# Performance work log

Hardware: AMD Instinct MI355X
Metric: run time of the kernel (lower is better)

The kernel has to match this reference:

```python
import jax, jax.numpy as jnp
import numpy as np

N = 50000      # nodes / stations
E = 600000     # edges
IN = 16        # in_channels
ED = 8         # edge_dim
HID = 128      # hidden
H = 4          # heads
C = HID // H   # 32 per-head channels
EMB = HID // 2 # station embedding dim
FEAT = HID - EMB
SLOPE = 0.2    # GATv2 LeakyReLU negative slope


def setup_inputs() -> dict:
    key = jax.random.key(0)
    ks = jax.random.split(key, 32)
    r = lambda i, shape, s=0.05: (jax.random.normal(ks[i], shape, jnp.float32) * s)
    inp = {
        "x": jax.random.normal(ks[0], (N, IN), jnp.float32),
        "node_idx": jax.random.randint(ks[1], (N,), 0, N),
        "edge_index": jax.random.randint(ks[2], (2, E), 0, N),
        "edge_attr": jax.random.normal(ks[3], (E, ED), jnp.float32),
        # params
        "emb": r(4, (N, EMB)),
        "W_in": r(5, (IN, FEAT)), "b_in": jnp.zeros((FEAT,), jnp.float32),
        # conv1 (GATv2: lin_l, lin_r, lin_edge, att, out bias)
        "Wl1": r(6, (HID, HID)), "bl1": jnp.zeros((HID,), jnp.float32),
        "Wr1": r(7, (HID, HID)), "br1": jnp.zeros((HID,), jnp.float32),
        "We1": r(8, (ED, HID)),  "be1": jnp.zeros((HID,), jnp.float32),
        "att1": r(9, (H, C)),    "bo1": jnp.zeros((HID,), jnp.float32),
        # conv2
        "Wl2": r(10, (HID, HID)), "bl2": jnp.zeros((HID,), jnp.float32),
        "Wr2": r(11, (HID, HID)), "br2": jnp.zeros((HID,), jnp.float32),
        "We2": r(12, (ED, HID)),  "be2": jnp.zeros((HID,), jnp.float32),
        "att2": r(13, (H, C)),    "bo2": jnp.zeros((HID,), jnp.float32),
        # layer norms
        "g1": jnp.ones((HID,), jnp.float32), "beta1": jnp.zeros((HID,), jnp.float32),
        "g2": jnp.ones((HID,), jnp.float32), "beta2": jnp.zeros((HID,), jnp.float32),
        # output head
        "W_out": r(14, (HID, 1)), "b_out": jnp.zeros((1,), jnp.float32),
    }
    return inp


def _gatv2(x, src, dst, ea, Wl, bl, Wr, br, We, be, att, bo):
    # x: [N,HID] -> per-head projections [N,H,C]
    xl = (x @ Wl + bl).reshape(-1, H, C)   # source transform
    xr = (x @ Wr + br).reshape(-1, H, C)   # target transform
    ee = (ea @ We + be).reshape(-1, H, C)  # edge transform [E,H,C]
    s = jax.nn.leaky_relu(xl[src] + xr[dst] + ee, SLOPE)  # [E,H,C]
    logit = jnp.einsum('ehc,hc->eh', s, att)              # [E,H]
    # segment softmax over destination node
    amax = jax.lax.stop_gradient(jax.ops.segment_max(logit, dst, num_segments=N))
    amax = jnp.where(jnp.isfinite(amax), amax, 0.0)
    ex = jnp.exp(logit - amax[dst])
    den = jax.ops.segment_sum(ex, dst, num_segments=N)
    alpha = ex / den[dst]                                  # [E,H]
    out = jax.ops.segment_sum(xl[src] * alpha[..., None], dst, num_segments=N)
    return out.reshape(-1, HID) + bo


def _ln(x, g, b):
    mu = x.mean(-1, keepdims=True)
    v = ((x - mu) ** 2).mean(-1, keepdims=True)
    return (x - mu) * jax.lax.rsqrt(v + 1e-5) * g + b


def reference(x, node_idx, edge_index, edge_attr, emb, W_in, b_in,
              Wl1, bl1, Wr1, br1, We1, be1, att1, bo1,
              Wl2, bl2, Wr2, br2, We2, be2, att2, bo2,
              g1, beta1, g2, beta2, W_out, b_out):
    src, dst = edge_index[0], edge_index[1]
    feat = jax.nn.relu(x @ W_in + b_in)                       # [N,FEAT]
    z = jnp.concatenate([feat, emb[node_idx]], axis=-1)       # [N,HID]
    h = jax.nn.relu(_gatv2(z, src, dst, edge_attr, Wl1, bl1, Wr1, br1, We1, be1, att1, bo1))
    z = _ln(z + h, g1, beta1)
    h = jax.nn.relu(_gatv2(z, src, dst, edge_attr, Wl2, bl2, Wr2, br2, We2, be2, att2, bo2))
    z = _ln(z + h, g2, beta2)
    return (z @ W_out + b_out).squeeze(-1)                    # [N]
```

## Files before the change

kernel.cpp:

```cpp
#include <hip/hip_runtime.h>
#include <hip/hip_bf16.h>

#define NN 50000
#define NE 600000
#define IND 16
#define EDD 8
#define HIDD 128
#define NH 4
#define CC 32
#define EMBD 64
#define FEATD 64
#define NB_SCAN ((NN + 255) / 256)

typedef __hip_bfloat16 bf16;
typedef __attribute__((ext_vector_type(8))) short bshort8;
typedef __attribute__((ext_vector_type(4))) float floatx4;

__device__ __forceinline__ float b2f(bf16 v) { return __bfloat162float(v); }

__device__ __forceinline__ unsigned short f2bu(float f) {
    unsigned int u = __float_as_uint(f);
    u += 0x7fffu + ((u >> 16) & 1u);
    return (unsigned short)(u >> 16);
}

template <bool F32>
__device__ __forceinline__ float LD(const void* p, long long i) {
    if constexpr (F32) return ((const float*)p)[i];
    else return __bfloat162float(((const bf16*)p)[i]);
}

__global__ void k_init0(int* __restrict__ cnt, int* __restrict__ deg) {
    int i = blockIdx.x * blockDim.x + threadIdx.x;
    if (i == 0) *cnt = 0;
    if (i < NN) deg[i] = 0;
}

__global__ void k_detect(const unsigned short* __restrict__ x, int nhalf, int* __restrict__ cnt) {
    __shared__ int c;
    if (threadIdx.x == 0) c = 0;
    __syncthreads();
    int i = blockIdx.x * blockDim.x + threadIdx.x;
    int hits = 0;
    for (; i < nhalf; i += gridDim.x * blockDim.x)
        if ((x[i] & 0x7F80u) == 0x7F80u) hits++;
    if (hits) atomicAdd(&c, hits);
    __syncthreads();
    if (threadIdx.x == 0 && c) atomicAdd(cnt, c);
}

__device__ __forceinline__ bool is_f32(const int* cnt) { return *cnt > 8; }

__global__ void k_hist(const int* __restrict__ ei, int* __restrict__ deg, int* __restrict__ rank) {
    int e = blockIdx.x * blockDim.x + threadIdx.x;
    if (e < NE) rank[e] = atomicAdd(&deg[ei[NE + e]], 1);
}

__global__ void k_scan1(const int* __restrict__ deg, int* __restrict__ off,
                        int* __restrict__ bsum) {
    __shared__ int tile[256];
    int t = threadIdx.x;
    int gid = blockIdx.x * 256 + t;
    int v = (gid < NN) ? deg[gid] : 0;
    tile[t] = v;
    __syncthreads();
    #pragma unroll
    for (int o = 1; o < 256; o <<= 1) {
        int u = (t >= o) ? tile[t - o] : 0;
        __syncthreads();
        tile[t] += u;
        __syncthreads();
    }
    if (gid < NN) off[gid] = tile[t] - v;
    if (t == 255) bsum[blockIdx.x] = tile[255];
}
__global__ void k_scan2(int* __restrict__ bsum) {
    __shared__ int tile[256];
    int t = threadIdx.x;
    int v = (t < NB_SCAN) ? bsum[t] : 0;
    tile[t] = v;
    __syncthreads();
    #pragma unroll
    for (int o = 1; o < 256; o <<= 1) {
        int u = (t >= o) ? tile[t - o] : 0;
        __syncthreads();
        tile[t] += u;
        __syncthreads();
    }
    if (t < NB_SCAN) bsum[t] = tile[t] - v;
}
__global__ void k_scan3(int* __restrict__ off, const int* __restrict__ bsum) {
    int gid = blockIdx.x * 256 + threadIdx.x;
    if (gid < NN) off[gid] += bsum[blockIdx.x];
    if (gid == 0) off[NN] = NE;
}

template <bool F32>
__device__ void fill_impl(const int* __restrict__ ei, const int* __restrict__ off,
                          const int* __restrict__ rank, int* __restrict__ esrc,
                          uint4* __restrict__ ea8, const void* ea) {
    int e = blockIdx.x * blockDim.x + threadIdx.x;
    if (e >= NE) return;
    int slot = off[ei[NE + e]] + rank[e];
    esrc[slot] = ei[e];
    unsigned int w[4];
    #pragma unroll
    for (int d = 0; d < 4; d++) {
        unsigned int lo = f2bu(LD<F32>(ea, (long long)e * EDD + 2 * d));
        unsigned int hi = f2bu(LD<F32>(ea, (long long)e * EDD + 2 * d + 1));
        w[d] = lo | (hi << 16);
    }
    uint4 v; v.x = w[0]; v.y = w[1]; v.z = w[2]; v.w = w[3];
    ea8[slot] = v;
}
__global__ void k_fill(const int* cnt, const int* ei, const int* off, const int* rank,
                       int* esrc, uint4* ea8, const void* ea) {
    if (is_f32(cnt)) fill_impl<true>(ei, off, rank, esrc, ea8, ea);
    else             fill_impl<false>(ei, off, rank, esrc, ea8, ea);
}

template <bool F32>
__device__ void build_z_impl(const void* x, const int* __restrict__ node_idx, const void* emb,
                             const void* W_in, const void* b_in, bf16* __restrict__ zb) {
    int n = blockIdx.x, t = threadIdx.x;
    float val;
    if (t < FEATD) {
        float acc = LD<F32>(b_in, t);
        #pragma unroll
        for (int k = 0; k < IND; k++)
            acc += LD<F32>(x, (long long)n * IND + k) * LD<F32>(W_in, k * FEATD + t);
        val = fmaxf(acc, 0.f);
    } else {
        val = LD<F32>(emb, (long long)node_idx[n] * EMBD + (t - FEATD));
    }
    zb[n * HIDD + t] = __float2bfloat16(val);
}
__global__ void k_build_z(const int* cnt, const void* x, const int* node_idx, const void* emb,
                          const void* W_in, const void* b_in, bf16* zb) {
    if (is_f32(cnt)) build_z_impl<true>(x, node_idx, emb, W_in, b_in, zb);
    else             build_z_impl<false>(x, node_idx, emb, W_in, b_in, zb);
}

template <bool F32>
__device__ void prepw_impl(const void* Wl1, const void* bl1, const void* Wr1, const void* br1,
                           const void* Wl2, const void* bl2, const void* Wr2, const void* br2,
                           bf16* __restrict__ wbT, float* __restrict__ bias) {
    int layer = blockIdx.x >> 8;
    int n = blockIdx.x & 255;
    int k = threadIdx.x;
    const void* W = layer ? (n < HIDD ? Wl2 : Wr2) : (n < HIDD ? Wl1 : Wr1);
    const void* b = layer ? (n < HIDD ? bl2 : br2) : (n < HIDD ? bl1 : br1);
    int nn = n & (HIDD - 1);
    wbT[(layer * 256 + n) * HIDD + k] = __float2bfloat16(LD<F32>(W, k * HIDD + nn));
    if (k == 0) bias[layer * 256 + n] = LD<F32>(b, nn);
}
__global__ void k_prepw(const int* cnt,
                        const void* Wl1, const void* bl1, const void* Wr1, const void* br1,
                        const void* Wl2, const void* bl2, const void* Wr2, const void* br2,
                        bf16* wbT, float* bias) {
    if (is_f32(cnt)) prepw_impl<true>(Wl1, bl1, Wr1, br1, Wl2, bl2, Wr2, br2, wbT, bias);
    else             prepw_impl<false>(Wl1, bl1, Wr1, br1, Wl2, bl2, Wr2, br2, wbT, bias);
}

__global__ __launch_bounds__(256) void k_projmm(const bf16* __restrict__ zb,
                                                const bf16* __restrict__ wbT,
                                                const float* __restrict__ bias,
                                                bf16* __restrict__ xl, bf16* __restrict__ xr) {
    int wave = threadIdx.x >> 6, lane = threadIdx.x & 63;
    int m0 = blockIdx.x * 64;
    int n0 = wave * 64;
    int l15 = lane & 15, q = lane >> 4;
    bshort8 bfr[4][4];
    #pragma unroll
    for (int j = 0; j < 4; j++)
        #pragma unroll
        for (int s = 0; s < 4; s++)
            bfr[j][s] = *(const bshort8*)(wbT + ((n0 + j * 16 + l15) << 7) + s * 32 + q * 8);
    float bv[4];
    #pragma unroll
    for (int j = 0; j < 4; j++) bv[j] = bias[n0 + j * 16 + l15];
    #pragma unroll
    for (int mi = 0; mi < 4; mi++) {
        const bf16* arow = zb + ((long long)(m0 + mi * 16 + l15) << 7) + q * 8;
        floatx4 acc0 = {0.f, 0.f, 0.f, 0.f}, acc1 = acc0, acc2 = acc0, acc3 = acc0;
        #pragma unroll
        for (int s = 0; s < 4; s++) {
            bshort8 a = *(const bshort8*)(arow + s * 32);
            acc0 = __builtin_amdgcn_mfma_f32_16x16x32_bf16(a, bfr[0][s], acc0, 0, 0, 0);
            acc1 = __builtin_amdgcn_mfma_f32_16x16x32_bf16(a, bfr[1][s], acc1, 0, 0, 0);
            acc2 = __builtin_amdgcn_mfma_f32_16x16x32_bf16(a, bfr[2][s], acc2, 0, 0, 0);
            acc3 = __builtin_amdgcn_mfma_f32_16x16x32_bf16(a, bfr[3][s], acc3, 0, 0, 0);
        }
        floatx4 accs[4] = {acc0, acc1, acc2, acc3};
        #pragma unroll
        for (int j = 0; j < 4; j++) {
            int colg = n0 + j * 16 + l15;
            bf16* dst = (colg < HIDD) ? (xl + colg) : (xr + (colg - HIDD));
            #pragma unroll
            for (int r = 0; r < 4; r++) {
                int rowc = m0 + mi * 16 + q * 4 + r;
                if (rowc < NN) dst[(long long)rowc << 7] = __float2bfloat16(accs[j][r] + bv[j]);
            }
        }
    }
}

template <bool F32, bool LAST>
__device__ void gat_impl(const int* __restrict__ off, const int* __restrict__ esrc,
                         const uint4* __restrict__ ea8,
                         const void* We, const void* be, const void* att,
                         const bf16* __restrict__ xl, const bf16* __restrict__ xr,
                         const void* bo, bf16* __restrict__ zb,
                         const void* g, const void* beta,
                         const void* Wo, const void* bout, void* out) {
    int wave = threadIdx.x >> 6;
    int half = (threadIdx.x >> 5) & 1;
    int lane5 = threadIdx.x & 31;
    int n = blockIdx.x * 8 + wave * 2 + half;
    int c0 = lane5 << 2;
    float wv[EDD][4], at[4], bev[4];
    #pragma unroll
    for (int d = 0; d < EDD; d++)
        #pragma unroll
        for (int j = 0; j < 4; j++) wv[d][j] = LD<F32>(We, d * HIDD + c0 + j);
    #pragma unroll
    for (int j = 0; j < 4; j++) {
        at[j] = LD<F32>(att, c0 + j);
        bev[j] = LD<F32>(be, c0 + j);
    }
    uint2 xru = *(const uint2*)(xr + ((long long)n << 7) + c0);
    float xrv[4];
    xrv[0] = __uint_as_float(xru.x << 16);
    xrv[1] = __uint_as_float(xru.x & 0xffff0000u);
    xrv[2] = __uint_as_float(xru.y << 16);
    xrv[3] = __uint_as_float(xru.y & 0xffff0000u);
    int lo = off[n], hi = off[n + 1];
    float acc[4] = {0.f, 0.f, 0.f, 0.f};
    float den = 0.f;
    if (lo < hi) {
        int src = esrc[lo];
        uint4 eu = ea8[lo];
        uint2 xu = *(const uint2*)(xl + ((long long)src << 7) + c0);
        for (int i = lo; i < hi; i++) {
            int ip = (i + 1 < hi) ? i + 1 : i;
            int src_n = esrc[ip];
            uint4 eu_n = ea8[ip];
            uint2 xu_n = *(const uint2*)(xl + ((long long)src_n << 7) + c0);
            float e[8];
            e[0] = __uint_as_float(eu.x << 16); e[1] = __uint_as_float(eu.x & 0xffff0000u);
            e[2] = __uint_as_float(eu.y << 16); e[3] = __uint_as_float(eu.y & 0xffff0000u);
            e[4] = __uint_as_float(eu.z << 16); e[5] = __uint_as_float(eu.z & 0xffff0000u);
            e[6] = __uint_as_float(eu.w << 16); e[7] = __uint_as_float(eu.w & 0xffff0000u);
            float xv[4];
            xv[0] = __uint_as_float(xu.x << 16);
            xv[1] = __uint_as_float(xu.x & 0xffff0000u);
            xv[2] = __uint_as_float(xu.y << 16);
            xv[3] = __uint_as_float(xu.y & 0xffff0000u);
            float ls = 0.f;
            #pragma unroll
            for (int j = 0; j < 4; j++) {
                float ee = bev[j];
                #pragma unroll
                for (int d = 0; d < EDD; d++) ee += e[d] * wv[d][j];
                float s = xv[j] + xrv[j] + ee;
                s = fmaxf(s, 0.2f * s);
                ls += s * at[j];
            }
            ls += __shfl_xor(ls, 1);
            ls += __shfl_xor(ls, 2);
            ls += __shfl_xor(ls, 4);
            float ex = __expf(ls);
            #pragma unroll
            for (int j = 0; j < 4; j++) acc[j] += ex * xv[j];
            den += ex;
            src = src_n; eu = eu_n; xu = xu_n;
        }
    }
    float inv = (den > 0.f) ? 1.0f / den : 0.f;
    uint2 zu = *(const uint2*)(zb + ((long long)n << 7) + c0);
    float zv[4];
    zv[0] = __uint_as_float(zu.x << 16);
    zv[1] = __uint_as_float(zu.x & 0xffff0000u);
    zv[2] = __uint_as_float(zu.y << 16);
    zv[3] = __uint_as_float(zu.y & 0xffff0000u);
    float v[4];
    float s = 0.f;
    #pragma unroll
    for (int j = 0; j < 4; j++) {
        float hv = fmaxf(acc[j] * inv + LD<F32>(bo, c0 + j), 0.f);
        v[j] = zv[j] + hv;
        s += v[j];
    }
    #pragma unroll
    for (int m = 16; m; m >>= 1) s += __shfl_xor(s, m);
    float mu = s * (1.f / HIDD);
    float s2 = 0.f;
    float dv[4];
    #pragma unroll
    for (int j = 0; j < 4; j++) { dv[j] = v[j] - mu; s2 += dv[j] * dv[j]; }
    #pragma unroll
    for (int m = 16; m; m >>= 1) s2 += __shfl_xor(s2, m);
    float rs = rsqrtf(s2 * (1.f / HIDD) + 1e-5f);
    float o[4];
    #pragma unroll
    for (int j = 0; j < 4; j++)
        o[j] = dv[j] * rs * LD<F32>(g, c0 + j) + LD<F32>(beta, c0 + j);
    if constexpr (!LAST) {
        uint2 pk;
        pk.x = (unsigned int)f2bu(o[0]) | ((unsigned int)f2bu(o[1]) << 16);
        pk.y = (unsigned int)f2bu(o[2]) | ((unsigned int)f2bu(o[3]) << 16);
        *(uint2*)(zb + ((long long)n << 7) + c0) = pk;
    } else {
        float po = 0.f;
        #pragma unroll
        for (int j = 0; j < 4; j++) po += o[j] * LD<F32>(Wo, c0 + j);
        #pragma unroll
        for (int m = 16; m; m >>= 1) po += __shfl_xor(po, m);
        if (lane5 == 0) {
            float r = po + LD<F32>(bout, 0);
            if constexpr (F32) ((float*)out)[n] = r;
            else               ((bf16*)out)[n] = __float2bfloat16(r);
        }
    }
}
__global__ void k_gat(const int* cnt, const int* off, const int* esrc, const uint4* ea8,
                      const void* We, const void* be, const void* att,
                      const bf16* xl, const bf16* xr, const void* bo, bf16* zb,
                      const void* g, const void* beta) {
    if (is_f32(cnt)) gat_impl<true, false>(off, esrc, ea8, We, be, att, xl, xr, bo, zb, g, beta, nullptr, nullptr, nullptr);
    else             gat_impl<false, false>(off, esrc, ea8, We, be, att, xl, xr, bo, zb, g, beta, nullptr, nullptr, nullptr);
}
__global__ void k_gat_last(const int* cnt, const int* off, const int* esrc, const uint4* ea8,
                           const void* We, const void* be, const void* att,
                           const bf16* xl, const bf16* xr, const void* bo, bf16* zb,
                           const void* g, const void* beta,
                           const void* Wo, const void* bout, void* out) {
    if (is_f32(cnt)) gat_impl<true, true>(off, esrc, ea8, We, be, att, xl, xr, bo, zb, g, beta, Wo, bout, out);
    else             gat_impl<false, true>(off, esrc, ea8, We, be, att, xl, xr, bo, zb, g, beta, Wo, bout, out);
}

extern "C" void kernel_launch(void* const* d_in, const int* in_sizes, int n_in,
                              void* d_out, int out_size, void* d_ws, size_t ws_size,
                              hipStream_t stream) {
    const void* x        = d_in[0];
    const int*  node_idx = (const int*)d_in[1];
    const int*  ei       = (const int*)d_in[2];
    const void* ea       = d_in[3];
    const void* emb      = d_in[4];
    const void* W_in     = d_in[5];
    const void* b_in     = d_in[6];
    const void* Wl1 = d_in[7];  const void* bl1 = d_in[8];
    const void* Wr1 = d_in[9];  const void* br1 = d_in[10];
    const void* We1 = d_in[11]; const void* be1 = d_in[12];
    const void* att1 = d_in[13]; const void* bo1 = d_in[14];
    const void* Wl2 = d_in[15]; const void* bl2 = d_in[16];
    const void* Wr2 = d_in[17]; const void* br2 = d_in[18];
    const void* We2 = d_in[19]; const void* be2 = d_in[20];
    const void* att2 = d_in[21]; const void* bo2 = d_in[22];
    const void* g1 = d_in[23]; const void* beta1 = d_in[24];
    const void* g2 = d_in[25]; const void* beta2 = d_in[26];
    const void* W_out = d_in[27]; const void* b_out = d_in[28];

    int*   cnt  = (int*)d_ws;
    uint4* ea8  = (uint4*)((char*)d_ws + 256);
    bf16*  zb   = (bf16*)(ea8 + NE);
    bf16*  xl   = zb + NN * HIDD;
    bf16*  xr   = xl + NN * HIDD;
    bf16*  wbT  = xr + NN * HIDD;
    float* bias = (float*)(wbT + 2 * 256 * HIDD);
    int*   off  = (int*)(bias + 2 * 256);
    int*   deg  = off + NN + 1;
    int*   rank = deg + NN;
    int*   esrc = rank + NE;
    int*   bsum = esrc + NE;

    int nhalf = in_sizes[0] < 65536 ? in_sizes[0] : 65536;
    k_init0<<<(NN + 255) / 256, 256, 0, stream>>>(cnt, deg);
    k_detect<<<64, 256, 0, stream>>>((const unsigned short*)x, nhalf, cnt);
    k_build_z<<<NN, 128, 0, stream>>>(cnt, x, node_idx, emb, W_in, b_in, zb);

    k_hist<<<(NE + 255) / 256, 256, 0, stream>>>(ei, deg, rank);
    k_scan1<<<NB_SCAN, 256, 0, stream>>>(deg, off, bsum);
    k_scan2<<<1, 256, 0, stream>>>(bsum);
    k_scan3<<<NB_SCAN, 256, 0, stream>>>(off, bsum);
    k_fill<<<(NE + 255) / 256, 256, 0, stream>>>(cnt, ei, off, rank, esrc, ea8, ea);

    k_prepw<<<512, HIDD, 0, stream>>>(cnt, Wl1, bl1, Wr1, br1, Wl2, bl2, Wr2, br2, wbT, bias);

    k_projmm<<<(NN + 63) / 64, 256, 0, stream>>>(zb, wbT, bias, xl, xr);
    k_gat<<<NN / 8, 256, 0, stream>>>(cnt, off, esrc, ea8, We1, be1, att1, xl, xr, bo1, zb, g1, beta1);

    k_projmm<<<(NN + 63) / 64, 256, 0, stream>>>(zb, wbT + 256 * HIDD, bias + 256, xl, xr);
    k_gat_last<<<NN / 8, 256, 0, stream>>>(cnt, off, esrc, ea8, We2, be2, att2, xl, xr, bo2, zb,
                                           g2, beta2, W_out, b_out, d_out);
}
```

Baseline: 422.8 us.

## Sort GAT nodes by degree, fuse prep kernels, halve projmm tile, pad edge arrays

Builds a degree-bucketed permutation of nodes (counting sort over degree clipped to 63) during the scan kernels. Both GAT layers then process nodes in that order, so the wave halves that share a block get similar edge counts and less idle time. The z-build and weight-prep kernels are merged into one launch, and projmm now computes 32 rows per block with A-fragments preloaded, giving more blocks. The edge arrays get a zero sentinel so the prefetch no longer needs a bounds clamp. The sorted order scatters zb/xr accesses and adds a few extra scan passes.

```diff
diff --git a/kernel.cpp b/kernel.cpp
--- a/kernel.cpp
+++ b/kernel.cpp
@@ -16,8 +16,6 @@
 typedef __attribute__((ext_vector_type(8))) short bshort8;
 typedef __attribute__((ext_vector_type(4))) float floatx4;
 
-__device__ __forceinline__ float b2f(bf16 v) { return __bfloat162float(v); }
-
 __device__ __forceinline__ unsigned short f2bu(float f) {
     unsigned int u = __float_as_uint(f);
     u += 0x7fffu + ((u >> 16) & 1u);
@@ -30,10 +28,11 @@
     else return __bfloat162float(((const bf16*)p)[i]);
 }
 
-__global__ void k_init0(int* __restrict__ cnt, int* __restrict__ deg) {
+__global__ void k_init0(int* __restrict__ cnt, int* __restrict__ deg, int* __restrict__ dcnt) {
     int i = blockIdx.x * blockDim.x + threadIdx.x;
     if (i == 0) *cnt = 0;
     if (i < NN) deg[i] = 0;
+    if (i < 64) dcnt[i] = 0;
 }
 
 __global__ void k_detect(const unsigned short* __restrict__ x, int nhalf, int* __restrict__ cnt) {
@@ -57,13 +56,22 @@
 }
 
 __global__ void k_scan1(const int* __restrict__ deg, int* __restrict__ off,
-                        int* __restrict__ bsum) {
+                        int* __restrict__ bsum, int* __restrict__ dcnt,
+                        int* __restrict__ rankd) {
     __shared__ int tile[256];
+    __shared__ int lh[64];
+    __shared__ int lbase[64];
     int t = threadIdx.x;
     int gid = blockIdx.x * 256 + t;
+    if (t < 64) lh[t] = 0;
+    __syncthreads();
     int v = (gid < NN) ? deg[gid] : 0;
+    int b = min(v, 63);
+    int lr = 0;
+    if (gid < NN) lr = atomicAdd(&lh[b], 1);
     tile[t] = v;
     __syncthreads();
+    if (t < 64) lbase[t] = lh[t] ? atomicAdd(&dcnt[t], lh[t]) : 0;
     #pragma unroll
     for (int o = 1; o < 256; o <<= 1) {
         int u = (t >= o) ? tile[t - o] : 0;
@@ -71,14 +79,21 @@
         tile[t] += u;
         __syncthreads();
     }
-    if (gid < NN) off[gid] = tile[t] - v;
+    if (gid < NN) {
+        off[gid] = tile[t] - v;
+        rankd[gid] = lbase[b] + lr;
+    }
     if (t == 255) bsum[blockIdx.x] = tile[255];
 }
-__global__ void k_scan2(int* __restrict__ bsum) {
+__global__ void k_scan2(int* __restrict__ bsum, int* __restrict__ dcnt,
+                        int* __restrict__ dbase) {
     __shared__ int tile[256];
+    __shared__ int d2[64];
     int t = threadIdx.x;
     int v = (t < NB_SCAN) ? bsum[t] : 0;
     tile[t] = v;
+    int dv = (t < 64) ? dcnt[t] : 0;
+    if (t < 64) d2[t] = dv;
     __syncthreads();
     #pragma unroll
     for (int o = 1; o < 256; o <<= 1) {
@@ -87,11 +102,25 @@
         tile[t] += u;
         __syncthreads();
     }
+    #pragma unroll
+    for (int o = 1; o < 64; o <<= 1) {
+        int u = (t >= o && t < 64) ? d2[t - o] : 0;
+        __syncthreads();
+        if (t < 64) d2[t] += u;
+        __syncthreads();
+    }
     if (t < NB_SCAN) bsum[t] = tile[t] - v;
-}
-__global__ void k_scan3(int* __restrict__ off, const int* __restrict__ bsum) {
+    if (t < 64) dbase[t] = d2[t] - dv;
+}
+__global__ void k_scan3(int* __restrict__ off, const int* __restrict__ bsum,
+                        const int* __restrict__ deg, const int* __restrict__ rankd,
+                        const int* __restrict__ dbase, int* __restrict__ perm) {
     int gid = blockIdx.x * 256 + threadIdx.x;
-    if (gid < NN) off[gid] += bsum[blockIdx.x];
+    if (gid < NN) {
+        off[gid] += bsum[blockIdx.x];
+        int b = min(deg[gid], 63);
+        perm[dbase[b] + rankd[gid]] = gid;
+    }
     if (gid == 0) off[NN] = NE;
 }
 
@@ -101,6 +130,11 @@
                           uint4* __restrict__ ea8, const void* ea) {
     int e = blockIdx.x * blockDim.x + threadIdx.x;
     if (e >= NE) return;
+    if (e == 0) {
+        esrc[NE] = 0;
+        uint4 z; z.x = 0; z.y = 0; z.z = 0; z.w = 0;
+        ea8[NE] = z;
+    }
     int slot = off[ei[NE + e]] + rank[e];
     esrc[slot] = ei[e];
     unsigned int w[4];
@@ -120,46 +154,45 @@
 }
 
 template <bool F32>
-__device__ void build_z_impl(const void* x, const int* __restrict__ node_idx, const void* emb,
-                             const void* W_in, const void* b_in, bf16* __restrict__ zb) {
-    int n = blockIdx.x, t = threadIdx.x;
-    float val;
-    if (t < FEATD) {
-        float acc = LD<F32>(b_in, t);
-        #pragma unroll
-        for (int k = 0; k < IND; k++)
-            acc += LD<F32>(x, (long long)n * IND + k) * LD<F32>(W_in, k * FEATD + t);
-        val = fmaxf(acc, 0.f);
+__device__ void bzpw_impl(const void* x, const int* __restrict__ node_idx, const void* emb,
+                          const void* W_in, const void* b_in, bf16* __restrict__ zb,
+                          const void* Wl1, const void* bl1, const void* Wr1, const void* br1,
+                          const void* Wl2, const void* bl2, const void* Wr2, const void* br2,
+                          bf16* __restrict__ wbT, float* __restrict__ bias) {
+    int t = threadIdx.x;
+    if (blockIdx.x < NN) {
+        int n = blockIdx.x;
+        float val;
+        if (t < FEATD) {
+            float acc = LD<F32>(b_in, t);
+            #pragma unroll
+            for (int k = 0; k < IND; k++)
+                acc += LD<F32>(x, (long long)n * IND + k) * LD<F32>(W_in, k * FEATD + t);
+            val = fmaxf(acc, 0.f);
+        } else {
+            val = LD<F32>(emb, (long long)node_idx[n] * EMBD + (t - FEATD));
+        }
+        zb[n * HIDD + t] = __float2bfloat16(val);
     } else {
-        val = LD<F32>(emb, (long long)node_idx[n] * EMBD + (t - FEATD));
-    }
-    zb[n * HIDD + t] = __float2bfloat16(val);
-}
-__global__ void k_build_z(const int* cnt, const void* x, const int* node_idx, const void* emb,
-                          const void* W_in, const void* b_in, bf16* zb) {
-    if (is_f32(cnt)) build_z_impl<true>(x, node_idx, emb, W_in, b_in, zb);
-    else             build_z_impl<false>(x, node_idx, emb, W_in, b_in, zb);
-}
-
-template <bool F32>
-__device__ void prepw_impl(const void* Wl1, const void* bl1, const void* Wr1, const void* br1,
-                           const void* Wl2, const void* bl2, const void* Wr2, const void* br2,
-                           bf16* __restrict__ wbT, float* __restrict__ bias) {
-    int layer = blockIdx.x >> 8;
-    int n = blockIdx.x & 255;
-    int k = threadIdx.x;
-    const void* W = layer ? (n < HIDD ? Wl2 : Wr2) : (n < HIDD ? Wl1 : Wr1);
-    const void* b = layer ? (n < HIDD ? bl2 : br2) : (n < HIDD ? bl1 : br1);
-    int nn = n & (HIDD - 1);
-    wbT[(layer * 256 + n) * HIDD + k] = __float2bfloat16(LD<F32>(W, k * HIDD + nn));
-    if (k == 0) bias[layer * 256 + n] = LD<F32>(b, nn);
-}
-__global__ void k_prepw(const int* cnt,
-                        const void* Wl1, const void* bl1, const void* Wr1, const void* br1,
-                        const void* Wl2, const void* bl2, const void* Wr2, const void* br2,
-                        bf16* wbT, float* bias) {
-    if (is_f32(cnt)) prepw_impl<true>(Wl1, bl1, Wr1, br1, Wl2, bl2, Wr2, br2, wbT, bias);
-    else             prepw_impl<false>(Wl1, bl1, Wr1, br1, Wl2, bl2, Wr2, br2, wbT, bias);
+        int bid = blockIdx.x - NN;
+        int layer = bid >> 8;
+        int n = bid & 255;
+        const void* W = layer ? (n < HIDD ? Wl2 : Wr2) : (n < HIDD ? Wl1 : Wr1);
+        const void* b = layer ? (n < HIDD ? bl2 : br2) : (n < HIDD ? bl1 : br1);
+        int nn = n & (HIDD - 1);
+        wbT[(layer * 256 + n) * HIDD + t] = __float2bfloat16(LD<F32>(W, t * HIDD + nn));
+        if (t == 0) bias[layer * 256 + n] = LD<F32>(b, nn);
+    }
+}
+__global__ void k_bzpw(const int* cnt, const void* x, const int* node_idx, const void* emb,
+                       const void* W_in, const void* b_in, bf16* zb,
+                       const void* Wl1, const void* bl1, const void* Wr1, const void* br1,
+                       const void* Wl2, const void* bl2, const void* Wr2, const void* br2,
+                       bf16* wbT, float* bias) {
+    if (is_f32(cnt)) bzpw_impl<true>(x, node_idx, emb, W_in, b_in, zb, Wl1, bl1, Wr1, br1,
+                                     Wl2, bl2, Wr2, br2, wbT, bias);
+    else             bzpw_impl<false>(x, node_idx, emb, W_in, b_in, zb, Wl1, bl1, Wr1, br1,
+                                      Wl2, bl2, Wr2, br2, wbT, bias);
 }
 
 __global__ __launch_bounds__(256) void k_projmm(const bf16* __restrict__ zb,
@@ -167,7 +200,7 @@
                                                 const float* __restrict__ bias,
                                                 bf16* __restrict__ xl, bf16* __restrict__ xr) {
     int wave = threadIdx.x >> 6, lane = threadIdx.x & 63;
-    int m0 = blockIdx.x * 64;
+    int m0 = blockIdx.x * 32;
     int n0 = wave * 64;
     int l15 = lane & 15, q = lane >> 4;
     bshort8 bfr[4][4];
@@ -179,13 +212,19 @@
     float bv[4];
     #pragma unroll
     for (int j = 0; j < 4; j++) bv[j] = bias[n0 + j * 16 + l15];
-    #pragma unroll
-    for (int mi = 0; mi < 4; mi++) {
-        const bf16* arow = zb + ((long long)(m0 + mi * 16 + l15) << 7) + q * 8;
+    const bf16* arow0 = zb + ((m0 + l15) << 7) + q * 8;
+    const bf16* arow1 = arow0 + (16 << 7);
+    bshort8 a0[4], a1[4];
+    #pragma unroll
+    for (int s = 0; s < 4; s++) a0[s] = *(const bshort8*)(arow0 + s * 32);
+    #pragma unroll
+    for (int s = 0; s < 4; s++) a1[s] = *(const bshort8*)(arow1 + s * 32);
+    #pragma unroll
+    for (int mi = 0; mi < 2; mi++) {
         floatx4 acc0 = {0.f, 0.f, 0.f, 0.f}, acc1 = acc0, acc2 = acc0, acc3 = acc0;
         #pragma unroll
         for (int s = 0; s < 4; s++) {
-            bshort8 a = *(const bshort8*)(arow + s * 32);
+            bshort8 a = mi ? a1[s] : a0[s];
             acc0 = __builtin_amdgcn_mfma_f32_16x16x32_bf16(a, bfr[0][s], acc0, 0, 0, 0);
             acc1 = __builtin_amdgcn_mfma_f32_16x16x32_bf16(a, bfr[1][s], acc1, 0, 0, 0);
             acc2 = __builtin_amdgcn_mfma_f32_16x16x32_bf16(a, bfr[2][s], acc2, 0, 0, 0);
@@ -199,14 +238,15 @@
             #pragma unroll
             for (int r = 0; r < 4; r++) {
                 int rowc = m0 + mi * 16 + q * 4 + r;
-                if (rowc < NN) dst[(long long)rowc << 7] = __float2bfloat16(accs[j][r] + bv[j]);
+                if (rowc < NN) dst[rowc << 7] = __float2bfloat16(accs[j][r] + bv[j]);
             }
         }
     }
 }
 
 template <bool F32, bool LAST>
-__device__ void gat_impl(const int* __restrict__ off, const int* __restrict__ esrc,
+__device__ void gat_impl(const int* __restrict__ perm,
+                         const int* __restrict__ off, const int* __restrict__ esrc,
                          const uint4* __restrict__ ea8,
                          const void* We, const void* be, const void* att,
                          const bf16* __restrict__ xl, const bf16* __restrict__ xr,
@@ -216,7 +256,7 @@
     int wave = threadIdx.x >> 6;
     int half = (threadIdx.x >> 5) & 1;
     int lane5 = threadIdx.x & 31;
-    int n = blockIdx.x * 8 + wave * 2 + half;
+    int n = perm[blockIdx.x * 8 + wave * 2 + half];
     int c0 = lane5 << 2;
     float wv[EDD][4], at[4], bev[4];
     #pragma unroll
@@ -228,7 +268,7 @@
         at[j] = LD<F32>(att, c0 + j);
         bev[j] = LD<F32>(be, c0 + j);
     }
-    uint2 xru = *(const uint2*)(xr + ((long long)n << 7) + c0);
+    uint2 xru = *(const uint2*)(xr + (n << 7) + c0);
     float xrv[4];
     xrv[0] = __uint_as_float(xru.x << 16);
     xrv[1] = __uint_as_float(xru.x & 0xffff0000u);
@@ -240,12 +280,11 @@
     if (lo < hi) {
         int src = esrc[lo];
         uint4 eu = ea8[lo];
-        uint2 xu = *(const uint2*)(xl + ((long long)src << 7) + c0);
+        uint2 xu = *(const uint2*)(xl + (src << 7) + c0);
         for (int i = lo; i < hi; i++) {
-            int ip = (i + 1 < hi) ? i + 1 : i;
-            int src_n = esrc[ip];
-            uint4 eu_n = ea8[ip];
-            uint2 xu_n = *(const uint2*)(xl + ((long long)src_n << 7) + c0);
+            int src_n = esrc[i + 1];
+            uint4 eu_n = ea8[i + 1];
+            uint2 xu_n = *(const uint2*)(xl + (src_n << 7) + c0);
             float e[8];
             e[0] = __uint_as_float(eu.x << 16); e[1] = __uint_as_float(eu.x & 0xffff0000u);
             e[2] = __uint_as_float(eu.y << 16); e[3] = __uint_as_float(eu.y & 0xffff0000u);
@@ -277,7 +316,7 @@
         }
     }
     float inv = (den > 0.f) ? 1.0f / den : 0.f;
-    uint2 zu = *(const uint2*)(zb + ((long long)n << 7) + c0);
+    uint2 zu = *(const uint2*)(zb + (n << 7) + c0);
     float zv[4];
     zv[0] = __uint_as_float(zu.x << 16);
     zv[1] = __uint_as_float(zu.x & 0xffff0000u);
@@ -309,7 +348,7 @@
         uint2 pk;
         pk.x = (unsigned int)f2bu(o[0]) | ((unsigned int)f2bu(o[1]) << 16);
         pk.y = (unsigned int)f2bu(o[2]) | ((unsigned int)f2bu(o[3]) << 16);
-        *(uint2*)(zb + ((long long)n << 7) + c0) = pk;
+        *(uint2*)(zb + (n << 7) + c0) = pk;
     } else {
         float po = 0.f;
         #pragma unroll
@@ -323,20 +362,20 @@
         }
     }
 }
-__global__ void k_gat(const int* cnt, const int* off, const int* esrc, const uint4* ea8,
-                      const void* We, const void* be, const void* att,
+__global__ void k_gat(const int* cnt, const int* perm, const int* off, const int* esrc,
+                      const uint4* ea8, const void* We, const void* be, const void* att,
                       const bf16* xl, const bf16* xr, const void* bo, bf16* zb,
                       const void* g, const void* beta) {
-    if (is_f32(cnt)) gat_impl<true, false>(off, esrc, ea8, We, be, att, xl, xr, bo, zb, g, beta, nullptr, nullptr, nullptr);
-    else             gat_impl<false, false>(off, esrc, ea8, We, be, att, xl, xr, bo, zb, g, beta, nullptr, nullptr, nullptr);
-}
-__global__ void k_gat_last(const int* cnt, const int* off, const int* esrc, const uint4* ea8,
-                           const void* We, const void* be, const void* att,
+    if (is_f32(cnt)) gat_impl<true, false>(perm, off, esrc, ea8, We, be, att, xl, xr, bo, zb, g, beta, nullptr, nullptr, nullptr);
+    else             gat_impl<false, false>(perm, off, esrc, ea8, We, be, att, xl, xr, bo, zb, g, beta, nullptr, nullptr, nullptr);
+}
+__global__ void k_gat_last(const int* cnt, const int* perm, const int* off, const int* esrc,
+                           const uint4* ea8, const void* We, const void* be, const void* att,
                            const bf16* xl, const bf16* xr, const void* bo, bf16* zb,
                            const void* g, const void* beta,
                            const void* Wo, const void* bout, void* out) {
-    if (is_f32(cnt)) gat_impl<true, true>(off, esrc, ea8, We, be, att, xl, xr, bo, zb, g, beta, Wo, bout, out);
-    else             gat_impl<false, true>(off, esrc, ea8, We, be, att, xl, xr, bo, zb, g, beta, Wo, bout, out);
+    if (is_f32(cnt)) gat_impl<true, true>(perm, off, esrc, ea8, We, be, att, xl, xr, bo, zb, g, beta, Wo, bout, out);
+    else             gat_impl<false, true>(perm, off, esrc, ea8, We, be, att, xl, xr, bo, zb, g, beta, Wo, bout, out);
 }
 
 extern "C" void kernel_launch(void* const* d_in, const int* in_sizes, int n_in,
@@ -361,36 +400,39 @@
     const void* g2 = d_in[25]; const void* beta2 = d_in[26];
     const void* W_out = d_in[27]; const void* b_out = d_in[28];
 
-    int*   cnt  = (int*)d_ws;
-    uint4* ea8  = (uint4*)((char*)d_ws + 256);
-    bf16*  zb   = (bf16*)(ea8 + NE);
-    bf16*  xl   = zb + NN * HIDD;
-    bf16*  xr   = xl + NN * HIDD;
-    bf16*  wbT  = xr + NN * HIDD;
-    float* bias = (float*)(wbT + 2 * 256 * HIDD);
-    int*   off  = (int*)(bias + 2 * 256);
-    int*   deg  = off + NN + 1;
-    int*   rank = deg + NN;
-    int*   esrc = rank + NE;
-    int*   bsum = esrc + NE;
+    int*   cnt   = (int*)d_ws;
+    uint4* ea8   = (uint4*)((char*)d_ws + 256);
+    bf16*  zb    = (bf16*)(ea8 + NE + 4);
+    bf16*  xl    = zb + NN * HIDD;
+    bf16*  xr    = xl + NN * HIDD;
+    bf16*  wbT   = xr + NN * HIDD;
+    float* bias  = (float*)(wbT + 2 * 256 * HIDD);
+    int*   off   = (int*)(bias + 512);
+    int*   deg   = off + NN + 1;
+    int*   rank  = deg + NN;
+    int*   rankd = rank + NE;
+    int*   perm  = rankd + NN;
+    int*   esrc  = perm + NN;
+    int*   bsum  = esrc + NE + 4;
+    int*   dcnt  = bsum + 256;
+    int*   dbase = dcnt + 64;
 
     int nhalf = in_sizes[0] < 65536 ? in_sizes[0] : 65536;
-    k_init0<<<(NN + 255) / 256, 256, 0, stream>>>(cnt, deg);
+    k_init0<<<(NN + 255) / 256, 256, 0, stream>>>(cnt, deg, dcnt);
     k_detect<<<64, 256, 0, stream>>>((const unsigned short*)x, nhalf, cnt);
-    k_build_z<<<NN, 128, 0, stream>>>(cnt, x, node_idx, emb, W_in, b_in, zb);
+    k_bzpw<<<NN + 512, HIDD, 0, stream>>>(cnt, x, node_idx, emb, W_in, b_in, zb,
+                                          Wl1, bl1, Wr1, br1, Wl2, bl2, Wr2, br2, wbT, bias);
 
     k_hist<<<(NE + 255) / 256, 256, 0, stream>>>(ei, deg, rank);
-    k_scan1<<<NB_SCAN, 256, 0, stream>>>(deg, off, bsum);
-    k_scan2<<<1, 256, 0, stream>>>(bsum);
-    k_scan3<<<NB_SCAN, 256, 0, stream>>>(off, bsum);
+    k_scan1<<<NB_SCAN, 256, 0, stream>>>(deg, off, bsum, dcnt, rankd);
+    k_scan2<<<1, 256, 0, stream>>>(bsum, dcnt, dbase);
+    k_scan3<<<NB_SCAN, 256, 0, stream>>>(off, bsum, deg, rankd, dbase, perm);
     k_fill<<<(NE + 255) / 256, 256, 0, stream>>>(cnt, ei, off, rank, esrc, ea8, ea);
 
-    k_prepw<<<512, HIDD, 0, stream>>>(cnt, Wl1, bl1, Wr1, br1, Wl2, bl2, Wr2, br2, wbT, bias);
-
-    k_projmm<<<(NN + 63) / 64, 256, 0, stream>>>(zb, wbT, bias, xl, xr);
-    k_gat<<<NN / 8, 256, 0, stream>>>(cnt, off, esrc, ea8, We1, be1, att1, xl, xr, bo1, zb, g1, beta1);
-
-    k_projmm<<<(NN + 63) / 64, 256, 0, stream>>>(zb, wbT + 256 * HIDD, bias + 256, xl, xr);
-    k_gat_last<<<NN / 8, 256, 0, stream>>>(cnt, off, esrc, ea8, We2, be2, att2, xl, xr, bo2, zb,
+    k_projmm<<<(NN + 31) / 32, 256, 0, stream>>>(zb, wbT, bias, xl, xr);
+    k_gat<<<NN / 8, 256, 0, stream>>>(cnt, perm, off, esrc, ea8, We1, be1, att1, xl, xr, bo1, zb, g1, beta1);
+
+    k_projmm<<<(NN + 31) / 32, 256, 0, stream>>>(zb, wbT + 256 * HIDD, bias + 256, xl, xr);
+    k_gat_last<<<NN / 8, 256, 0, stream>>>(cnt, perm, off, esrc, ea8, We2, be2, att2, xl, xr, bo2, zb,
                                            g2, beta2, W_out, b_out, d_out);
 }
```

New measurement: 408.9 us. 1.03x faster.
